# Kernel optimization log

Hardware: AMD Instinct MI355X
Metric: run time of the kernel (lower is better)

The kernel has to match this reference:

```python
import jax, jax.numpy as jnp
import numpy as np

B, S, D_IN, D, L, H, Z, FUT, FF = 64, 512, 64, 512, 4, 8, 64, 96, 2048

def _ln(x, g, b, eps=1e-5):
    m = x.mean(-1, keepdims=True)
    v = ((x - m) ** 2).mean(-1, keepdims=True)
    return (x - m) / jnp.sqrt(v + eps) * g + b

def setup_inputs() -> dict:
    key = jax.random.key(0)
    ks = iter(jax.random.split(key, 48))
    def w(shape, s=0.02):
        return s * jax.random.normal(next(ks), shape, jnp.float32)
    inp = {
        'X': jax.random.normal(next(ks), (B, S, D_IN), jnp.float32),
        'eps': jax.random.normal(next(ks), (B, Z), jnp.float32),
        'u': jax.random.uniform(next(ks), (B, Z), jnp.float32, 0.0, 0.99),
        'choice': jax.random.uniform(next(ks), (B,), jnp.float32),
        'We': w((D, D_IN)), 'be': jnp.zeros((D,), jnp.float32),
        'Wqkv': w((L, 3 * D, D)), 'bqkv': jnp.zeros((L, 3 * D), jnp.float32),
        'Wo': w((L, D, D)), 'bo': jnp.zeros((L, D), jnp.float32),
        'ln1g': jnp.ones((L, D), jnp.float32), 'ln1b': jnp.zeros((L, D), jnp.float32),
        'W1': w((L, FF, D)), 'b1': jnp.zeros((L, FF), jnp.float32),
        'W2': w((L, D, FF)), 'b2': jnp.zeros((L, D), jnp.float32),
        'ln2g': jnp.ones((L, D), jnp.float32), 'ln2b': jnp.zeros((L, D), jnp.float32),
        'Wm': w((Z, D)), 'bm': jnp.zeros((Z,), jnp.float32),
        'Wlv': w((Z, D)), 'blv': jnp.zeros((Z,), jnp.float32),
        'Wsc': w((Z, D)), 'bsc': jnp.zeros((Z,), jnp.float32),
        'Wsh': w((Z, D)), 'bsh': 0.1 * jnp.ones((Z,), jnp.float32),
        'pi_params': jnp.array([3.0, 0.01], jnp.float32),
        'Wfc1': w((128, Z)), 'bfc1': jnp.zeros((128,), jnp.float32),
        'Wfc2': w((500, 128)), 'bfc2': jnp.zeros((500,), jnp.float32),
        'Wout': w((FUT, 500)), 'bout': jnp.zeros((FUT,), jnp.float32),
        'Wfin': w((FUT, FUT)), 'bfin': jnp.zeros((FUT,), jnp.float32),
    }
    return inp

def reference(X, eps, u, choice, We, be, Wqkv, bqkv, Wo, bo, ln1g, ln1b,
              W1, b1, W2, b2, ln2g, ln2b, Wm, bm, Wlv, blv, Wsc, bsc,
              Wsh, bsh, pi_params, Wfc1, bfc1, Wfc2, bfc2, Wout, bout,
              Wfin, bfin):
    b, s, _ = X.shape
    d = We.shape[0]
    dh = d // H
    nlayers = Wqkv.shape[0]
    # embedding
    x = X @ We.T + be                                   # [B,S,D]
    for l in range(nlayers):
        qkv = x @ Wqkv[l].T + bqkv[l]                   # [B,S,3D]
        q, k, v = jnp.split(qkv, 3, axis=-1)
        hd = lambda t: t.reshape(b, s, H, dh).transpose(0, 2, 1, 3)
        q, k, v = hd(q), hd(k), hd(v)                   # [B,H,S,dh]
        sc = jnp.einsum('bhqd,bhkd->bhqk', q, k) / np.sqrt(dh).astype(np.float32)
        a = jax.nn.softmax(sc, axis=-1)
        o = jnp.einsum('bhqk,bhkd->bhqd', a, v).transpose(0, 2, 1, 3).reshape(b, s, d)
        o = o @ Wo[l].T + bo[l]
        x = _ln(x + o, ln1g[l], ln1b[l])                # post-norm (torch default)
        ff = jax.nn.relu(x @ W1[l].T + b1[l]) @ W2[l].T + b2[l]
        x = _ln(x + ff, ln2g[l], ln2b[l])
    h = x[:, -1]                                        # transformer_out[-1] after (S,B,D) permute
    mean = h @ Wm.T + bm
    logvar = h @ Wlv.T + blv
    scale = jnp.exp(h @ Wsc.T + bsc)
    shape = h @ Wsh.T + bsh
    # mixture reparameterization (vectorized mask-select, replaces per-sample loop)
    pi0 = jax.nn.softmax(pi_params)[0]
    z_gauss = mean + eps * jnp.exp(0.5 * logvar)
    z_gpd = scale / shape * ((1.0 - u) ** (-shape) - 1.0)
    z = jnp.where((choice < pi0)[:, None], z_gauss, z_gpd)
    # decoder (dropout = eval mode / identity)
    dlt = jax.nn.relu(z @ Wfc1.T + bfc1)
    dlt = jax.nn.relu(dlt @ Wfc2.T + bfc2)
    out = dlt @ Wout.T + bout
    rec = out @ Wfin.T + bfin
    return rec, mean, logvar, scale, shape
```

## Files before the change

### kernel.cpp

```cpp
#include <hip/hip_runtime.h>
#include <hip/hip_bf16.h>
#include <stdint.h>

typedef __bf16 bf16_t;
typedef __bf16 bf16x8 __attribute__((ext_vector_type(8)));
typedef __bf16 bf16x4 __attribute__((ext_vector_type(4)));
typedef float f32x4 __attribute__((ext_vector_type(4)));
typedef unsigned int u32;
typedef unsigned short u16;

static constexpr int Bd = 64, Sd = 512, Dd = 512, Hd = 8, Ld = 4, FFd = 2048, Zd = 64, FUTd = 96;

__device__ __forceinline__ int xcd_swz(int flat, int nwg) {
    int q = nwg >> 3, r = nwg & 7;
    int xcd = flat & 7, idx = flat >> 3;
    return (xcd < r ? xcd * (q + 1) : r * (q + 1) + (xcd - r) * q) + idx;
}

__device__ __forceinline__ void gld_lds16(const bf16_t* g, bf16_t* l) {
    __builtin_amdgcn_global_load_lds(
        (const __attribute__((address_space(1))) u32*)g,
        (__attribute__((address_space(3))) u32*)l, 16, 0, 0);
}

__global__ void cvt_k(const float* __restrict__ in, bf16_t* __restrict__ out, int n4) {
    int i = blockIdx.x * 256 + threadIdx.x;
    if (i >= n4) return;
    float4 v = ((const float4*)in)[i];
    bf16x4 o;
    o[0] = (bf16_t)v.x; o[1] = (bf16_t)v.y; o[2] = (bf16_t)v.z; o[3] = (bf16_t)v.w;
    ((bf16x4*)out)[i] = o;
}

template<bool RELU, bool HAS_RES>
__global__ __launch_bounds__(256, 3) void gemm_k(
    const bf16_t* __restrict__ A, const bf16_t* __restrict__ W,
    const float* __restrict__ bias, const bf16_t* __restrict__ res,
    bf16_t* __restrict__ outb, int M, int N, int K)
{
    __shared__ __align__(16) bf16_t As[128 * 64];
    __shared__ __align__(16) bf16_t Bs[128 * 64];
    const int tid  = threadIdx.x;
    const int lane = tid & 63;
    const int w    = tid >> 6;
    const int wr   = w >> 1, wc = w & 1;
    const int nwg  = gridDim.x * gridDim.y;
    const int flat = xcd_swz(blockIdx.y * gridDim.x + blockIdx.x, nwg);
    const int bm   = (flat / gridDim.x) * 128;
    const int bn   = (flat % gridDim.x) * 128;
    const int r15  = lane & 15;
    const int g4   = lane >> 4;

    int rs[4], cs[4];
#pragma unroll
    for (int j = 0; j < 4; ++j) {
        int slot = w * 4 + j;
        int r = slot * 8 + (lane >> 3);
        rs[j] = r;
        cs[j] = (lane & 7) ^ (r & 7);
    }

    f32x4 acc[4][4];
#pragma unroll
    for (int m = 0; m < 4; ++m)
#pragma unroll
        for (int n = 0; n < 4; ++n) acc[m][n] = (f32x4){0.f, 0.f, 0.f, 0.f};

    for (int kt = 0; kt < K; kt += 64) {
#pragma unroll
        for (int j = 0; j < 4; ++j) {
            int slot = w * 4 + j;
            gld_lds16(A + (size_t)(bm + rs[j]) * K + kt + cs[j] * 8, As + slot * 512);
            gld_lds16(W + (size_t)(bn + rs[j]) * K + kt + cs[j] * 8, Bs + slot * 512);
        }
        __syncthreads();
#pragma unroll
        for (int kk = 0; kk < 2; ++kk) {
            bf16x8 af[4], bfr[4];
#pragma unroll
            for (int m = 0; m < 4; ++m) {
                int r = wr * 64 + m * 16 + r15;
                int c = (kk * 4 + g4) ^ (r & 7);
                af[m] = *(const bf16x8*)(As + r * 64 + c * 8);
            }
#pragma unroll
            for (int n = 0; n < 4; ++n) {
                int r = wc * 64 + n * 16 + r15;
                int c = (kk * 4 + g4) ^ (r & 7);
                bfr[n] = *(const bf16x8*)(Bs + r * 64 + c * 8);
            }
#pragma unroll
            for (int m = 0; m < 4; ++m)
#pragma unroll
                for (int n = 0; n < 4; ++n)
                    acc[m][n] = __builtin_amdgcn_mfma_f32_16x16x32_bf16(af[m], bfr[n], acc[m][n], 0, 0, 0);
        }
        __syncthreads();
    }

    const int row0 = bm + wr * 64 + g4 * 4;
    const int col0 = bn + wc * 64 + r15;
#pragma unroll
    for (int n = 0; n < 4; ++n) {
        const int col = col0 + n * 16;
        const float bv = bias[col];
#pragma unroll
        for (int m = 0; m < 4; ++m) {
#pragma unroll
            for (int j = 0; j < 4; ++j) {
                const int row = row0 + m * 16 + j;
                size_t off = (size_t)row * N + col;
                float v = acc[m][n][j] + bv;
                if (HAS_RES) v += (float)res[off];
                if (RELU) v = fmaxf(v, 0.f);
                outb[off] = (bf16_t)v;
            }
        }
    }
}

__global__ __launch_bounds__(512, 2) void attn_k(const bf16_t* __restrict__ qkv, bf16_t* __restrict__ out) {
    const int bid  = xcd_swz(blockIdx.x, gridDim.x);
    const int qblk = bid & 3;
    const int h    = (bid >> 2) & 7;
    const int bb   = bid >> 5;
    const int tid  = threadIdx.x;
    const int lane = tid & 63;
    const int w    = tid >> 6;
    const int r15  = lane & 15;
    const int g4   = lane >> 4;

    __shared__ __align__(16) bf16_t Ks[64 * 64];
    __shared__ __align__(16) bf16_t VT[64 * 72];
    __shared__ __align__(16) bf16_t Ps[8][16 * 72];

    const size_t base = (size_t)bb * Sd * 1536;
    const int q0 = qblk * 128 + w * 16;

    bf16x8 qf[2];
    {
        const int qr = q0 + r15;
#pragma unroll
        for (int kk = 0; kk < 2; ++kk)
            qf[kk] = *(const bf16x8*)(qkv + base + (size_t)qr * 1536 + h * 64 + kk * 32 + g4 * 8);
    }

    f32x4 oacc[4];
#pragma unroll
    for (int dg = 0; dg < 4; ++dg) oacc[dg] = (f32x4){0.f, 0.f, 0.f, 0.f};
    float lrun[4] = {0.f, 0.f, 0.f, 0.f};

    for (int kv0 = 0; kv0 < Sd; kv0 += 64) {
        __syncthreads();
        {
            const int r = tid >> 3, c = tid & 7;
            const int cl = c ^ (r & 7);
            gld_lds16(qkv + base + (size_t)(kv0 + r) * 1536 + 512 + h * 64 + cl * 8,
                      Ks + (w * 64) * 8);
        }
        if (tid < 256) {
            const int r2 = tid >> 3, c = tid & 7;
            const bf16_t* vc = qkv + base + (size_t)(kv0 + 2 * r2) * 1536 + 1024 + h * 64 + c * 8;
            uint4 va = *(const uint4*)vc;
            uint4 vb = *(const uint4*)(vc + 1536);
            const u16* pa = (const u16*)&va;
            const u16* pb = (const u16*)&vb;
            const int rx = (2 * r2) ^ (c << 3);
#pragma unroll
            for (int e = 0; e < 8; ++e) {
                u32 wv = (u32)pa[e] | ((u32)pb[e] << 16);
                *(u32*)(VT + (c * 8 + e) * 72 + rx) = wv;
            }
        }
        __syncthreads();

        f32x4 sreg[4];
#pragma unroll
        for (int cg = 0; cg < 4; ++cg) {
            f32x4 a = (f32x4){0.f, 0.f, 0.f, 0.f};
#pragma unroll
            for (int kk = 0; kk < 2; ++kk) {
                int rk = cg * 16 + r15;
                int ck = (kk * 4 + g4) ^ (rk & 7);
                bf16x8 kf = *(const bf16x8*)(Ks + rk * 64 + ck * 8);
                a = __builtin_amdgcn_mfma_f32_16x16x32_bf16(qf[kk], kf, a, 0, 0, 0);
            }
            sreg[cg] = a * 0.125f;
        }

        float rsum[4] = {0.f, 0.f, 0.f, 0.f};
#pragma unroll
        for (int cg = 0; cg < 4; ++cg)
#pragma unroll
            for (int j = 0; j < 4; ++j) {
                float pv = __expf(sreg[cg][j]);
                sreg[cg][j] = pv;
                rsum[j] += pv;
            }
#pragma unroll
        for (int j = 0; j < 4; ++j) {
#pragma unroll
            for (int o = 1; o < 16; o <<= 1) rsum[j] += __shfl_xor(rsum[j], o);
            lrun[j] += rsum[j];
        }

#pragma unroll
        for (int cg = 0; cg < 4; ++cg)
#pragma unroll
            for (int j = 0; j < 4; ++j)
                Ps[w][(g4 * 4 + j) * 72 + cg * 16 + r15] = (bf16_t)sreg[cg][j];

        bf16x8 pf[2];
#pragma unroll
        for (int kk = 0; kk < 2; ++kk)
            pf[kk] = *(const bf16x8*)(&Ps[w][0] + r15 * 72 + kk * 32 + g4 * 8);

#pragma unroll
        for (int dg = 0; dg < 4; ++dg)
#pragma unroll
            for (int kk = 0; kk < 2; ++kk) {
                const int d = dg * 16 + r15;
                const int kvx = (kk * 32 + g4 * 8) ^ (((d >> 3) & 7) << 3);
                bf16x8 vf = *(const bf16x8*)(VT + d * 72 + kvx);
                oacc[dg] = __builtin_amdgcn_mfma_f32_16x16x32_bf16(pf[kk], vf, oacc[dg], 0, 0, 0);
            }
    }

#pragma unroll
    for (int dg = 0; dg < 4; ++dg)
#pragma unroll
        for (int j = 0; j < 4; ++j) {
            int row = q0 + g4 * 4 + j;
            out[(size_t)(bb * Sd + row) * Dd + h * 64 + dg * 16 + r15] = (bf16_t)(oacc[dg][j] / lrun[j]);
        }
}

__global__ __launch_bounds__(256) void ln_k(const bf16_t* __restrict__ in, const float* __restrict__ gg,
                                            const float* __restrict__ bb, bf16_t* __restrict__ outb) {
    const int w = threadIdx.x >> 6, lane = threadIdx.x & 63;
    const size_t row = (size_t)blockIdx.x * 4 + w;
    const int col = lane * 8;
    bf16x8 xv = *(const bf16x8*)(in + row * 512 + col);
    float x[8];
#pragma unroll
    for (int i = 0; i < 8; ++i) x[i] = (float)xv[i];
    float s = 0.f, sq = 0.f;
#pragma unroll
    for (int i = 0; i < 8; ++i) { s += x[i]; sq += x[i] * x[i]; }
#pragma unroll
    for (int o = 1; o < 64; o <<= 1) { s += __shfl_xor(s, o); sq += __shfl_xor(sq, o); }
    const float mean = s * (1.f / 512.f);
    const float var  = sq * (1.f / 512.f) - mean * mean;
    const float rstd = rsqrtf(var + 1e-5f);
    const float4 g0 = *(const float4*)(gg + col), g1 = *(const float4*)(gg + col + 4);
    const float4 b0 = *(const float4*)(bb + col), b1 = *(const float4*)(bb + col + 4);
    const float g[8] = {g0.x, g0.y, g0.z, g0.w, g1.x, g1.y, g1.z, g1.w};
    const float b[8] = {b0.x, b0.y, b0.z, b0.w, b1.x, b1.y, b1.z, b1.w};
    bf16x8 ob;
#pragma unroll
    for (int i = 0; i < 8; ++i) ob[i] = (bf16_t)((x[i] - mean) * rstd * g[i] + b[i]);
    *(bf16x8*)(outb + row * 512 + col) = ob;
}

__global__ __launch_bounds__(256) void head_k(const bf16_t* __restrict__ xsp,
                                              const float* __restrict__ Wm, const float* __restrict__ bm,
                                              const float* __restrict__ Wlv, const float* __restrict__ blv,
                                              const float* __restrict__ Wsc, const float* __restrict__ bsc,
                                              const float* __restrict__ Wsh, const float* __restrict__ bsh,
                                              const float* __restrict__ pi, const float* __restrict__ eps,
                                              const float* __restrict__ u, const float* __restrict__ choice,
                                              float* __restrict__ outp, float* __restrict__ z) {
    const int b = blockIdx.x;
    const int tid = threadIdx.x;
    __shared__ __align__(16) float hl[512];
    __shared__ float dots[4][64];
    const bf16_t* h = xsp + (size_t)(b * Sd + (Sd - 1)) * Dd;
    for (int i = tid; i < 512; i += 256) hl[i] = (float)h[i];
    __syncthreads();
    const int head = tid >> 6, zi = tid & 63;
    const float* Wp = head == 0 ? Wm : head == 1 ? Wlv : head == 2 ? Wsc : Wsh;
    const float* bp = head == 0 ? bm : head == 1 ? blv : head == 2 ? bsc : bsh;
    const float4* w4 = (const float4*)(Wp + zi * 512);
    const float4* h4 = (const float4*)hl;
    float acc = 0.f;
    for (int k = 0; k < 128; ++k) {
        float4 x = h4[k], y = w4[k];
        acc += x.x * y.x + x.y * y.y + x.z * y.z + x.w * y.w;
    }
    acc += bp[zi];
    float outv = (head == 2) ? __expf(acc) : acc;
    dots[head][zi] = outv;
    outp[FUTd * Bd + head * (Bd * Zd) + b * Zd + zi] = outv;
    __syncthreads();
    if (tid < 64) {
        float mean = dots[0][tid], lv = dots[1][tid], sc = dots[2][tid], sh = dots[3][tid];
        float a0 = pi[0], a1 = pi[1];
        float mx = fmaxf(a0, a1);
        float e0 = __expf(a0 - mx), e1 = __expf(a1 - mx);
        float pi0 = e0 / (e0 + e1);
        float zg = mean + eps[b * 64 + tid] * __expf(0.5f * lv);
        float uu = u[b * 64 + tid];
        float zp = sc / sh * (powf(1.f - uu, -sh) - 1.f);
        z[b * 64 + tid] = (choice[b] < pi0) ? zg : zp;
    }
}

template<bool RELU>
__global__ void sgemm_k(const float* __restrict__ A, const float* __restrict__ W,
                        const float* __restrict__ bias, float* __restrict__ outf,
                        int M, int N, int K) {
    int idx = blockIdx.x * 256 + threadIdx.x;
    if (idx >= M * N) return;
    int row = idx / N, col = idx - row * N;
    const float4* a4 = (const float4*)(A + (size_t)row * K);
    const float4* w4 = (const float4*)(W + (size_t)col * K);
    float acc = 0.f;
    for (int k = 0; k < (K >> 2); ++k) {
        float4 x = a4[k], y = w4[k];
        acc += x.x * y.x + x.y * y.y + x.z * y.z + x.w * y.w;
    }
    acc += bias[col];
    if (RELU) acc = fmaxf(acc, 0.f);
    outf[idx] = acc;
}

extern "C" void kernel_launch(void* const* d_in, const int* in_sizes, int n_in,
                              void* d_out, int out_size, void* d_ws, size_t ws_size,
                              hipStream_t stream) {
    const float* X      = (const float*)d_in[0];
    const float* eps    = (const float*)d_in[1];
    const float* u      = (const float*)d_in[2];
    const float* choice = (const float*)d_in[3];
    const float* We     = (const float*)d_in[4];
    const float* be     = (const float*)d_in[5];
    const float* Wqkv   = (const float*)d_in[6];
    const float* bqkv   = (const float*)d_in[7];
    const float* Wo     = (const float*)d_in[8];
    const float* bo     = (const float*)d_in[9];
    const float* ln1g   = (const float*)d_in[10];
    const float* ln1b   = (const float*)d_in[11];
    const float* W1     = (const float*)d_in[12];
    const float* b1     = (const float*)d_in[13];
    const float* W2     = (const float*)d_in[14];
    const float* b2     = (const float*)d_in[15];
    const float* ln2g   = (const float*)d_in[16];
    const float* ln2b   = (const float*)d_in[17];
    const float* Wm     = (const float*)d_in[18];
    const float* bm     = (const float*)d_in[19];
    const float* Wlv    = (const float*)d_in[20];
    const float* blv    = (const float*)d_in[21];
    const float* Wsc    = (const float*)d_in[22];
    const float* bsc    = (const float*)d_in[23];
    const float* Wsh    = (const float*)d_in[24];
    const float* bsh    = (const float*)d_in[25];
    const float* pip    = (const float*)d_in[26];
    const float* Wfc1   = (const float*)d_in[27];
    const float* bfc1   = (const float*)d_in[28];
    const float* Wfc2   = (const float*)d_in[29];
    const float* bfc2   = (const float*)d_in[30];
    const float* Wout   = (const float*)d_in[31];
    const float* bout   = (const float*)d_in[32];
    const float* Wfin   = (const float*)d_in[33];
    const float* bfin   = (const float*)d_in[34];
    float* outp = (float*)d_out;

    const int BS  = Bd * Sd;
    const int BSH = BS / 2;

    char* p = (char*)d_ws;
    auto alloc = [&](size_t bytes) { char* r = p; p += (bytes + 255) & ~(size_t)255; return r; };
    bf16_t* We_b   = (bf16_t*)alloc((size_t)Dd * 64 * 2);
    bf16_t* Wqkv_b = (bf16_t*)alloc((size_t)Ld * 3 * Dd * Dd * 2);
    bf16_t* Wo_b   = (bf16_t*)alloc((size_t)Ld * Dd * Dd * 2);
    bf16_t* W1_b   = (bf16_t*)alloc((size_t)Ld * FFd * Dd * 2);
    bf16_t* W2_b   = (bf16_t*)alloc((size_t)Ld * Dd * FFd * 2);
    bf16_t* Xb     = (bf16_t*)alloc((size_t)BS * 64 * 2);
    bf16_t* xa     = (bf16_t*)alloc((size_t)BS * Dd * 2);
    bf16_t* xpre   = (bf16_t*)alloc((size_t)BS * Dd * 2);
    bf16_t* sbuf   = (bf16_t*)alloc((size_t)BSH * FFd * 2);
    float*  zbuf   = (float*)alloc((size_t)Bd * Zd * 4);
    float*  d1     = (float*)alloc((size_t)Bd * 128 * 4);
    float*  d2     = (float*)alloc((size_t)Bd * 500 * 4);
    float*  o3     = (float*)alloc((size_t)Bd * FUTd * 4);
    size_t needed = (size_t)(p - (char*)d_ws);
    if (ws_size < needed) return;

    auto cg = [](int n4) { return (n4 + 255) / 256; };
    cvt_k<<<cg(Dd * 64 / 4), 256, 0, stream>>>(We, We_b, Dd * 64 / 4);
    cvt_k<<<cg(Ld * 3 * Dd * Dd / 4), 256, 0, stream>>>(Wqkv, Wqkv_b, Ld * 3 * Dd * Dd / 4);
    cvt_k<<<cg(Ld * Dd * Dd / 4), 256, 0, stream>>>(Wo, Wo_b, Ld * Dd * Dd / 4);
    cvt_k<<<cg(Ld * FFd * Dd / 4), 256, 0, stream>>>(W1, W1_b, Ld * FFd * Dd / 4);
    cvt_k<<<cg(Ld * Dd * FFd / 4), 256, 0, stream>>>(W2, W2_b, Ld * Dd * FFd / 4);
    cvt_k<<<cg(BS * 64 / 4), 256, 0, stream>>>(X, Xb, BS * 64 / 4);

    gemm_k<false, false><<<dim3(Dd / 128, BS / 128), 256, 0, stream>>>(
        Xb, We_b, be, nullptr, xa, BS, Dd, 64);

    bf16_t* attno = sbuf + (size_t)BSH * 1536;

    for (int l = 0; l < Ld; ++l) {
        for (int hb = 0; hb < 2; ++hb) {
            bf16_t* xa_h   = xa   + (size_t)hb * BSH * Dd;
            bf16_t* xpre_h = xpre + (size_t)hb * BSH * Dd;
            gemm_k<false, false><<<dim3(3 * Dd / 128, BSH / 128), 256, 0, stream>>>(
                xa_h, Wqkv_b + (size_t)l * 3 * Dd * Dd, bqkv + (size_t)l * 3 * Dd, nullptr,
                sbuf, BSH, 3 * Dd, Dd);
            attn_k<<<(Bd / 2) * Hd * (Sd / 128), 512, 0, stream>>>(sbuf, attno);
            gemm_k<false, true><<<dim3(Dd / 128, BSH / 128), 256, 0, stream>>>(
                attno, Wo_b + (size_t)l * Dd * Dd, bo + (size_t)l * Dd, xa_h,
                xpre_h, BSH, Dd, Dd);
        }
        ln_k<<<BS / 4, 256, 0, stream>>>(xpre, ln1g + (size_t)l * Dd, ln1b + (size_t)l * Dd, xa);
        for (int hb = 0; hb < 2; ++hb) {
            bf16_t* xa_h   = xa   + (size_t)hb * BSH * Dd;
            bf16_t* xpre_h = xpre + (size_t)hb * BSH * Dd;
            gemm_k<true, false><<<dim3(FFd / 128, BSH / 128), 256, 0, stream>>>(
                xa_h, W1_b + (size_t)l * FFd * Dd, b1 + (size_t)l * FFd, nullptr,
                sbuf, BSH, FFd, Dd);
            gemm_k<false, true><<<dim3(Dd / 128, BSH / 128), 256, 0, stream>>>(
                sbuf, W2_b + (size_t)l * Dd * FFd, b2 + (size_t)l * Dd, xa_h,
                xpre_h, BSH, Dd, FFd);
        }
        ln_k<<<BS / 4, 256, 0, stream>>>(xpre, ln2g + (size_t)l * Dd, ln2b + (size_t)l * Dd, xa);
    }

    head_k<<<Bd, 256, 0, stream>>>(xa, Wm, bm, Wlv, blv, Wsc, bsc, Wsh, bsh,
                                   pip, eps, u, choice, outp, zbuf);
    sgemm_k<true ><<<(Bd * 128 + 255) / 256, 256, 0, stream>>>(zbuf, Wfc1, bfc1, d1, Bd, 128, Zd);
    sgemm_k<true ><<<(Bd * 500 + 255) / 256, 256, 0, stream>>>(d1, Wfc2, bfc2, d2, Bd, 500, 128);
    sgemm_k<false><<<(Bd * FUTd + 255) / 256, 256, 0, stream>>>(d2, Wout, bout, o3, Bd, FUTd, 500);
    sgemm_k<false><<<(Bd * FUTd + 255) / 256, 256, 0, stream>>>(o3, Wfin, bfin, outp, Bd, FUTd, FUTd);
}
```

Baseline: 1.899 ms.

## Add 256x256-tile double-buffered GEMM kernel for QKV and FFN1 projections

Introduces a new 512-thread GEMM kernel with 256x256 output tiles, double-buffered LDS staging via direct global-to-LDS loads, XOR-swizzled layout, and interleaved prefetch within the MFMA loop. It replaces the 128x128 GEMM for the wide QKV and FFN up-projection GEMMs. This raises arithmetic intensity per block and overlaps loads with compute, at the cost of fewer blocks (less parallelism for the QKV grid of 6x64) and high register and LDS use per block.

```diff
diff --git a/kernel.cpp b/kernel.cpp
--- a/kernel.cpp
+++ b/kernel.cpp
@@ -30,6 +30,115 @@
     bf16x4 o;
     o[0] = (bf16_t)v.x; o[1] = (bf16_t)v.y; o[2] = (bf16_t)v.z; o[3] = (bf16_t)v.w;
     ((bf16x4*)out)[i] = o;
+}
+
+template<bool RELU>
+__global__ __launch_bounds__(512, 2) void gemm256_k(
+    const bf16_t* __restrict__ A, const bf16_t* __restrict__ W,
+    const float* __restrict__ bias, bf16_t* __restrict__ outb,
+    int M, int N, int K)
+{
+    __shared__ __align__(16) bf16_t sm[2][32768];
+    const int tid  = threadIdx.x;
+    const int lane = tid & 63;
+    const int wid  = tid >> 6;
+    const int wm   = wid >> 2, wn = wid & 3;
+    const int r15  = lane & 15;
+    const int g4   = lane >> 4;
+
+    const int nwg  = gridDim.x * gridDim.y;
+    const int flat = xcd_swz(blockIdx.y * gridDim.x + blockIdx.x, nwg);
+    const int bm   = (flat / gridDim.x) * 256;
+    const int bn   = (flat % gridDim.x) * 256;
+
+    auto stage_half = [&](int b, int h, int kt) {
+        const bf16_t* src = (h < 2) ? A : W;
+        const int rbase = ((h < 2) ? bm : bn) + ((h & 1) << 7);
+        bf16_t* dst = &sm[b][0] + h * 8192;
+#pragma unroll
+        for (int it = 0; it < 2; ++it) {
+            const int q = it * 512 + tid;
+            const int r = q >> 3, c = q & 7;
+            const int cl = c ^ (r & 7);
+            gld_lds16(src + (size_t)(rbase + r) * K + kt + cl * 8,
+                      dst + (it * 512 + wid * 64) * 8);
+        }
+    };
+
+    f32x4 acc[8][4];
+#pragma unroll
+    for (int i = 0; i < 8; ++i)
+#pragma unroll
+        for (int n = 0; n < 4; ++n) acc[i][n] = (f32x4){0.f, 0.f, 0.f, 0.f};
+
+    const int NT = K >> 6;
+#pragma unroll
+    for (int h = 0; h < 4; ++h) stage_half(0, h, 0);
+    __syncthreads();
+
+    bf16x8 bfr[4][2];
+    for (int t = 0; t < NT; ++t) {
+        const int cur = t & 1;
+        const bf16_t* Ah = &sm[cur][0] + wm * 8192;
+        const bf16_t* Bh = &sm[cur][0] + 16384 + (wn >> 1) * 8192;
+        const int ktn = (t + 1) << 6;
+        const bool pf = (t + 1 < NT);
+#pragma unroll
+        for (int p = 0; p < 4; ++p) {
+            if (p == 0) {
+#pragma unroll
+                for (int n = 0; n < 4; ++n)
+#pragma unroll
+                    for (int kk = 0; kk < 2; ++kk) {
+                        const int rl = (wn & 1) * 64 + n * 16 + r15;
+                        const int c = (kk * 4 + g4) ^ (rl & 7);
+                        bfr[n][kk] = *(const bf16x8*)(Bh + rl * 64 + c * 8);
+                    }
+            }
+            bf16x8 af[2][2];
+#pragma unroll
+            for (int ii = 0; ii < 2; ++ii)
+#pragma unroll
+                for (int kk = 0; kk < 2; ++kk) {
+                    const int rl = (p * 2 + ii) * 16 + r15;
+                    const int c = (kk * 4 + g4) ^ (rl & 7);
+                    af[ii][kk] = *(const bf16x8*)(Ah + rl * 64 + c * 8);
+                }
+            asm volatile("s_waitcnt lgkmcnt(0)" ::: "memory");
+            __builtin_amdgcn_s_barrier();
+            __builtin_amdgcn_sched_barrier(0);
+            if (pf) stage_half(cur ^ 1, p, ktn);
+            __builtin_amdgcn_s_setprio(1);
+#pragma unroll
+            for (int ii = 0; ii < 2; ++ii)
+#pragma unroll
+                for (int n = 0; n < 4; ++n)
+#pragma unroll
+                    for (int kk = 0; kk < 2; ++kk)
+                        acc[p * 2 + ii][n] = __builtin_amdgcn_mfma_f32_16x16x32_bf16(
+                            af[ii][kk], bfr[n][kk], acc[p * 2 + ii][n], 0, 0, 0);
+            __builtin_amdgcn_s_setprio(0);
+        }
+        asm volatile("s_waitcnt vmcnt(0)" ::: "memory");
+        __builtin_amdgcn_s_barrier();
+        __builtin_amdgcn_sched_barrier(0);
+    }
+
+#pragma unroll
+    for (int n = 0; n < 4; ++n) {
+        const int col = bn + wn * 64 + n * 16 + r15;
+        const float bv = bias[col];
+#pragma unroll
+        for (int i = 0; i < 8; ++i) {
+#pragma unroll
+            for (int jj = 0; jj < 4; ++jj) {
+                const int row = bm + wm * 128 + i * 16 + g4 * 4 + jj;
+                float v = acc[i][n][jj] + bv;
+                if (RELU) v = fmaxf(v, 0.f);
+                outb[(size_t)row * N + col] = (bf16_t)v;
+            }
+        }
+    }
 }
 
 template<bool RELU, bool HAS_RES>
@@ -402,8 +511,8 @@
         for (int hb = 0; hb < 2; ++hb) {
             bf16_t* xa_h   = xa   + (size_t)hb * BSH * Dd;
             bf16_t* xpre_h = xpre + (size_t)hb * BSH * Dd;
-            gemm_k<false, false><<<dim3(3 * Dd / 128, BSH / 128), 256, 0, stream>>>(
-                xa_h, Wqkv_b + (size_t)l * 3 * Dd * Dd, bqkv + (size_t)l * 3 * Dd, nullptr,
+            gemm256_k<false><<<dim3(3 * Dd / 256, BSH / 256), 512, 0, stream>>>(
+                xa_h, Wqkv_b + (size_t)l * 3 * Dd * Dd, bqkv + (size_t)l * 3 * Dd,
                 sbuf, BSH, 3 * Dd, Dd);
             attn_k<<<(Bd / 2) * Hd * (Sd / 128), 512, 0, stream>>>(sbuf, attno);
             gemm_k<false, true><<<dim3(Dd / 128, BSH / 128), 256, 0, stream>>>(
@@ -414,8 +523,8 @@
         for (int hb = 0; hb < 2; ++hb) {
             bf16_t* xa_h   = xa   + (size_t)hb * BSH * Dd;
             bf16_t* xpre_h = xpre + (size_t)hb * BSH * Dd;
-            gemm_k<true, false><<<dim3(FFd / 128, BSH / 128), 256, 0, stream>>>(
-                xa_h, W1_b + (size_t)l * FFd * Dd, b1 + (size_t)l * FFd, nullptr,
+            gemm256_k<true><<<dim3(FFd / 256, BSH / 256), 512, 0, stream>>>(
+                xa_h, W1_b + (size_t)l * FFd * Dd, b1 + (size_t)l * FFd,
                 sbuf, BSH, FFd, Dd);
             gemm_k<false, true><<<dim3(Dd / 128, BSH / 128), 256, 0, stream>>>(
                 sbuf, W2_b + (size_t)l * Dd * FFd, b2 + (size_t)l * Dd, xa_h,
```

After: 2.003 ms. +5.5%, slower.
